# Optimization experiments

Hardware: AMD Instinct MI355X
Metric: run time of the kernel (lower is better)

Reference implementation:

```python
import jax, jax.numpy as jnp
import numpy as np
import math

H = 1024   # d_model
N = 64     # state size; N//2 complex modes
L_LEN = 4096


def setup_inputs() -> dict:
    key = jax.random.key(0)
    k1, k2 = jax.random.split(key)
    # S4D init: log_dt uniform in [log(dt_min), log(dt_max)]
    log_dt = jax.random.uniform(k1, (H,), dtype=jnp.float32) * (
        math.log(0.1) - math.log(0.001)) + math.log(0.001)
    # C complex, stored as real view (channels=1, H, N/2, 2)
    C_real = jax.random.normal(k2, (1, H, N // 2, 2), dtype=jnp.float32)
    log_A_real = jnp.log(0.5 * jnp.ones((H, N // 2), dtype=jnp.float32))
    A_imag = math.pi * jnp.tile(jnp.arange(N // 2, dtype=jnp.float32), (H, 1))
    return {"log_dt": log_dt, "C_real": C_real, "log_A_real": log_A_real,
            "A_imag": A_imag, "L": L_LEN}


def reference(log_dt, C_real, log_A_real, A_imag, L):
    # materialize_parms
    dt = jnp.exp(log_dt)                                  # (H,)
    A = -jnp.exp(log_A_real) + 1j * A_imag                # (H, N/2) complex
    C = C_real[..., 0] + 1j * C_real[..., 1]              # (1, H, N/2) complex
    # discretize (bilinear)
    dtA = A * dt[:, None]                                 # (H, N/2)
    B = dt[:, None] / (1.0 - dtA / 2)                     # (H, N/2)
    dC = C * B                                            # (1, H, N/2)
    dA = (1.0 + dtA / 2) / (1.0 - dtA / 2)                # (H, N/2)
    # log-Vandermonde: K[c,h,l] = 2*Re sum_n dC[c,h,n] * dA[h,n]**l
    x = jnp.log(dA)                                       # (H, N/2) complex
    ls = jnp.arange(L)                                    # (L,)
    V = jnp.exp(x[..., None] * ls)                        # (H, N/2, L) complex
    K = 2.0 * jnp.real(jnp.einsum('chn,hnl->chl', dC, V)) # (1, H, L)
    return K
```

## Files before the change

### kernel.cpp

```cpp
#include <hip/hip_runtime.h>
#include <math.h>

#define MODES 32
#define BLOCK 256
#define TWO_PI 6.283185307179586f
#define INV_2PI 0.15915494309189535f

__device__ __forceinline__ float rfl(float x) {
    return __int_as_float(__builtin_amdgcn_readfirstlane(__float_as_int(x)));
}

__global__ __launch_bounds__(BLOCK) void s4d_kernel(
    const float* __restrict__ log_dt,
    const float* __restrict__ C_real,
    const float* __restrict__ log_A_real,
    const float* __restrict__ A_imag,
    float* __restrict__ out,
    int L)
{
    const int h   = blockIdx.x;
    const int tid = threadIdx.x;
    const int P   = L / BLOCK;

    __shared__ float4 s_c0[MODES];
    __shared__ float4 s_c1[MODES];

    if (tid < MODES) {
        const int n = tid;
        const float dt = __expf(log_dt[h]);
        const float ar = -__expf(log_A_real[h * MODES + n]);
        const float ai = A_imag[h * MODES + n];
        const float dtAr = ar * dt, dtAi = ai * dt;
        const float den_r = 1.0f - 0.5f * dtAr, den_i = -0.5f * dtAi;
        const float num_r = 1.0f + 0.5f * dtAr, num_i =  0.5f * dtAi;
        const float inv = 1.0f / (den_r * den_r + den_i * den_i);
        const float Br =  dt * den_r * inv;
        const float Bi = -dt * den_i * inv;
        const float Cr = C_real[(h * MODES + n) * 2 + 0];
        const float Ci = C_real[(h * MODES + n) * 2 + 1];
        const float dCr = Cr * Br - Ci * Bi;
        const float dCi = Cr * Bi + Ci * Br;
        const float dAr = (num_r * den_r + num_i * den_i) * inv;
        const float dAi = (num_i * den_r - num_r * den_i) * inv;
        const float xr  = 0.5f * __logf(dAr * dAr + dAi * dAi);
        const float rev = atan2f(dAi, dAr) * INV_2PI;

        const float S   = (float)BLOCK;
        const float mag = __expf(xr * S);
        const float t   = rev * S;
        const float fr  = t - rintf(t);
        float ws, wc;
        __sincosf(fr * TWO_PI, &ws, &wc);
        const float wr = mag * wc, wi = mag * ws;

        s_c0[n] = make_float4(xr, rev, 2.0f * dCr, 2.0f * dCi);
        s_c1[n] = make_float4(wr, wi, 2.0f * wr, -(mag * mag));
    }
    __syncthreads();

    float m0[MODES], m1[MODES];
    float aS[MODES], bS[MODES];
    float acc0 = 0.0f, acc1 = 0.0f;
    const float lf = (float)tid;

    #pragma unroll
    for (int n = 0; n < MODES; ++n) {
        const float4 c0 = s_c0[n];
        const float4 c1 = s_c1[n];
        const float er = __expf(c0.x * lf);
        const float t  = c0.y * lf;
        const float fr = t - rintf(t);
        float sn, cs;
        __sincosf(fr * TWO_PI, &sn, &cs);
        const float pr = er * cs, pi = er * sn;
        const float v0 = fmaf(c0.z, pr, -c0.w * pi);
        const float qr = fmaf(pr, c1.x, -pi * c1.y);
        const float qi = fmaf(pr, c1.y,  pi * c1.x);
        const float v1 = fmaf(c0.z, qr, -c0.w * qi);
        m0[n] = v0; m1[n] = v1;
        acc0 += v0; acc1 += v1;
        aS[n] = rfl(c1.z);
        bS[n] = rfl(c1.w);
    }

    float* outp = out + (size_t)h * (size_t)L + tid;
    outp[0] = acc0;
    if (P > 1) outp[BLOCK] = acc1;

    int p = 2;
    for (; p + 1 < P; p += 2) {
        float accA = 0.0f, accB = 0.0f;
        #pragma unroll
        for (int n = 0; n < MODES; ++n) {
            const float mA = fmaf(aS[n], m1[n], bS[n] * m0[n]);
            const float mB = fmaf(aS[n], mA,    bS[n] * m1[n]);
            accA += mA; accB += mB;
            m0[n] = mA; m1[n] = mB;
        }
        outp[(size_t)p * BLOCK]       = accA;
        outp[(size_t)(p + 1) * BLOCK] = accB;
    }
    if (p < P) {
        float accA = 0.0f;
        #pragma unroll
        for (int n = 0; n < MODES; ++n) {
            const float mA = fmaf(aS[n], m1[n], bS[n] * m0[n]);
            accA += mA;
            m0[n] = m1[n]; m1[n] = mA;
        }
        outp[(size_t)p * BLOCK] = accA;
    }
}

extern "C" void kernel_launch(void* const* d_in, const int* in_sizes, int n_in,
                              void* d_out, int out_size, void* d_ws, size_t ws_size,
                              hipStream_t stream) {
    const float* log_dt     = (const float*)d_in[0];
    const float* C_real     = (const float*)d_in[1];
    const float* log_A_real = (const float*)d_in[2];
    const float* A_imag     = (const float*)d_in[3];
    float* out = (float*)d_out;

    const int H = in_sizes[0];
    const int L = out_size / H;

    s4d_kernel<<<H, BLOCK, 0, stream>>>(log_dt, C_real, log_A_real, A_imag, out, L);
}
```

Before: 78.62 us.

## Compute Vandermonde sum as split-bf16 MFMA GEMM factored over 64x64 positions

Writes each position l as 64*i+j, so that dA^l factors into dA^(64i) * dA^j. The kernel builds two 64x32 complex factor matrices in LDS and evaluates the mode sum as a small matrix multiply on MFMA bf16 instructions. A hi/lo bf16 split with three cross products stands in for fp32 precision. This replaces the per-thread serial second-order recurrence over L with a fixed amount of matrix-core work. The risk is lost accuracy from the bf16 splitting and the dropped lo*lo term. The old recurrence kernel stays as a fallback when L is not 4096.

New measurement: 71.18 us. 9.5% less time.

```diff
diff --git a/kernel.cpp b/kernel.cpp
--- a/kernel.cpp
+++ b/kernel.cpp
@@ -5,28 +5,44 @@
 #define BLOCK 256
 #define TWO_PI 6.283185307179586f
 #define INV_2PI 0.15915494309189535f
-
-__device__ __forceinline__ float rfl(float x) {
-    return __int_as_float(__builtin_amdgcn_readfirstlane(__float_as_int(x)));
-}
-
-__global__ __launch_bounds__(BLOCK) void s4d_kernel(
+#define LROWW 36
+
+typedef __attribute__((ext_vector_type(8))) short bf16x8;
+typedef __attribute__((ext_vector_type(4))) float f32x4;
+
+__device__ __forceinline__ void split2(float a, float b, unsigned int& hi, unsigned int& lo) {
+    unsigned int ua = __float_as_uint(a);
+    unsigned int ra = ua + 0x7FFFu + ((ua >> 16) & 1u);
+    unsigned int ub = __float_as_uint(b);
+    unsigned int rb = ub + 0x7FFFu + ((ub >> 16) & 1u);
+    float ha = __uint_as_float(ra & 0xFFFF0000u);
+    float hb = __uint_as_float(rb & 0xFFFF0000u);
+    float la = a - ha, lb = b - hb;
+    unsigned int ula = __float_as_uint(la); ula += 0x7FFFu + ((ula >> 16) & 1u);
+    unsigned int ulb = __float_as_uint(lb); ulb += 0x7FFFu + ((ulb >> 16) & 1u);
+    hi = (ra >> 16) | (rb & 0xFFFF0000u);
+    lo = (ula >> 16) | (ulb & 0xFFFF0000u);
+}
+
+__global__ __launch_bounds__(BLOCK) void s4d_mfma(
     const float* __restrict__ log_dt,
     const float* __restrict__ C_real,
     const float* __restrict__ log_A_real,
     const float* __restrict__ A_imag,
-    float* __restrict__ out,
-    int L)
+    float* __restrict__ out)
 {
-    const int h   = blockIdx.x;
-    const int tid = threadIdx.x;
-    const int P   = L / BLOCK;
-
-    __shared__ float4 s_c0[MODES];
-    __shared__ float4 s_c1[MODES];
-
-    if (tid < MODES) {
-        const int n = tid;
+    __shared__ __align__(16) unsigned int sAhi[64 * LROWW];
+    __shared__ __align__(16) unsigned int sAlo[64 * LROWW];
+    __shared__ __align__(16) unsigned int sBhi[64 * LROWW];
+    __shared__ __align__(16) unsigned int sBlo[64 * LROWW];
+    __shared__ float s_xr[MODES], s_rev[MODES], s_xr64[MODES], s_rev64[MODES];
+    __shared__ float s_dcr[MODES], s_dci[MODES];
+
+    const int h = blockIdx.x;
+    const int t = threadIdx.x;
+
+    if (t < MODES) {
+        const int n = t;
         const float dt = __expf(log_dt[h]);
         const float ar = -__expf(log_A_real[h * MODES + n]);
         const float ai = A_imag[h * MODES + n];
@@ -44,69 +60,156 @@
         const float dAi = (num_i * den_r - num_r * den_i) * inv;
         const float xr  = 0.5f * __logf(dAr * dAr + dAi * dAi);
         const float rev = atan2f(dAi, dAr) * INV_2PI;
-
-        const float S   = (float)BLOCK;
+        s_xr[n]  = xr;
+        s_rev[n] = rev;
+        s_xr64[n] = 64.0f * xr;
+        float r64 = 64.0f * rev; r64 -= rintf(r64);
+        s_rev64[n] = r64;
+        s_dcr[n] = 2.0f * dCr;
+        s_dci[n] = 2.0f * dCi;
+    }
+    __syncthreads();
+
+    {
+        const int mode = t & 31;
+        const int i8   = t >> 5;
+        const float xr = s_xr[mode], rev = s_rev[mode];
+        const float xr64 = s_xr64[mode], rev64 = s_rev64[mode];
+        const float dcr = s_dcr[mode], dci = s_dci[mode];
+        #pragma unroll
+        for (int b = 0; b < 8; ++b) {
+            const int idx = i8 + b * 8;
+            const float f = (float)idx;
+            const int word = idx * LROWW + mode;
+            {
+                const float er = __expf(xr * f);
+                float ph = rev * f; ph -= rintf(ph);
+                float sn, cs; __sincosf(ph * TWO_PI, &sn, &cs);
+                unsigned int hi, lo;
+                split2(er * cs, er * sn, hi, lo);
+                sBhi[word] = hi; sBlo[word] = lo;
+            }
+            {
+                const float mag = __expf(xr64 * f);
+                float ph = rev64 * f; ph -= rintf(ph);
+                float sn, cs; __sincosf(ph * TWO_PI, &sn, &cs);
+                const float wr = mag * cs, wi = mag * sn;
+                const float pr  = dcr * wr - dci * wi;
+                const float pi2 = dcr * wi + dci * wr;
+                unsigned int hi, lo;
+                split2(pr, -pi2, hi, lo);
+                sAhi[word] = hi; sAlo[word] = lo;
+            }
+        }
+    }
+    __syncthreads();
+
+    const int wv   = t >> 6;
+    const int lane = t & 63;
+    const int c16  = lane & 15;
+    const int quad = lane >> 4;
+
+    const int arow = (wv * 16 + c16) * LROWW + quad * 4;
+    const bf16x8 ah0 = *(const bf16x8*)&sAhi[arow];
+    const bf16x8 ah1 = *(const bf16x8*)&sAhi[arow + 16];
+    const bf16x8 al0 = *(const bf16x8*)&sAlo[arow];
+    const bf16x8 al1 = *(const bf16x8*)&sAlo[arow + 16];
+
+    float* op = out + ((size_t)h << 12) + (size_t)(wv * 16 + quad * 4) * 64 + c16;
+
+    #pragma unroll
+    for (int nt = 0; nt < 4; ++nt) {
+        const int brow = (nt * 16 + c16) * LROWW + quad * 4;
+        const bf16x8 bh0 = *(const bf16x8*)&sBhi[brow];
+        const bf16x8 bh1 = *(const bf16x8*)&sBhi[brow + 16];
+        const bf16x8 bl0 = *(const bf16x8*)&sBlo[brow];
+        const bf16x8 bl1 = *(const bf16x8*)&sBlo[brow + 16];
+
+        f32x4 acc = {0.f, 0.f, 0.f, 0.f};
+        acc = __builtin_amdgcn_mfma_f32_16x16x32_bf16(ah0, bh0, acc, 0, 0, 0);
+        acc = __builtin_amdgcn_mfma_f32_16x16x32_bf16(ah1, bh1, acc, 0, 0, 0);
+        acc = __builtin_amdgcn_mfma_f32_16x16x32_bf16(ah0, bl0, acc, 0, 0, 0);
+        acc = __builtin_amdgcn_mfma_f32_16x16x32_bf16(ah1, bl1, acc, 0, 0, 0);
+        acc = __builtin_amdgcn_mfma_f32_16x16x32_bf16(al0, bh0, acc, 0, 0, 0);
+        acc = __builtin_amdgcn_mfma_f32_16x16x32_bf16(al1, bh1, acc, 0, 0, 0);
+
+        #pragma unroll
+        for (int r = 0; r < 4; ++r)
+            op[(size_t)r * 64 + nt * 16] = acc[r];
+    }
+}
+
+__global__ __launch_bounds__(BLOCK) void s4d_recur(
+    const float* __restrict__ log_dt, const float* __restrict__ C_real,
+    const float* __restrict__ log_A_real, const float* __restrict__ A_imag,
+    float* __restrict__ out, int L)
+{
+    const int h = blockIdx.x, tid = threadIdx.x;
+    const int P = L / BLOCK;
+    __shared__ float4 s_c0[MODES], s_c1[MODES];
+    if (tid < MODES) {
+        const int n = tid;
+        const float dt = __expf(log_dt[h]);
+        const float ar = -__expf(log_A_real[h * MODES + n]);
+        const float ai = A_imag[h * MODES + n];
+        const float dtAr = ar * dt, dtAi = ai * dt;
+        const float den_r = 1.0f - 0.5f * dtAr, den_i = -0.5f * dtAi;
+        const float num_r = 1.0f + 0.5f * dtAr, num_i = 0.5f * dtAi;
+        const float inv = 1.0f / (den_r * den_r + den_i * den_i);
+        const float Brr = dt * den_r * inv, Bii = -dt * den_i * inv;
+        const float Cr = C_real[(h * MODES + n) * 2 + 0];
+        const float Ci = C_real[(h * MODES + n) * 2 + 1];
+        const float dCr = Cr * Brr - Ci * Bii, dCi = Cr * Bii + Ci * Brr;
+        const float dAr = (num_r * den_r + num_i * den_i) * inv;
+        const float dAi = (num_i * den_r - num_r * den_i) * inv;
+        const float xr = 0.5f * __logf(dAr * dAr + dAi * dAi);
+        const float rev = atan2f(dAi, dAr) * INV_2PI;
+        const float S = (float)BLOCK;
         const float mag = __expf(xr * S);
-        const float t   = rev * S;
-        const float fr  = t - rintf(t);
-        float ws, wc;
-        __sincosf(fr * TWO_PI, &ws, &wc);
-        const float wr = mag * wc, wi = mag * ws;
-
+        float tt = rev * S; tt -= rintf(tt);
+        float ws, wc; __sincosf(tt * TWO_PI, &ws, &wc);
         s_c0[n] = make_float4(xr, rev, 2.0f * dCr, 2.0f * dCi);
-        s_c1[n] = make_float4(wr, wi, 2.0f * wr, -(mag * mag));
+        s_c1[n] = make_float4(mag * wc, mag * ws, 2.0f * mag * wc, -(mag * mag));
     }
     __syncthreads();
-
-    float m0[MODES], m1[MODES];
-    float aS[MODES], bS[MODES];
-    float acc0 = 0.0f, acc1 = 0.0f;
+    float m0[MODES], m1[MODES], aS[MODES], bS[MODES];
+    float acc0 = 0.f, acc1 = 0.f;
     const float lf = (float)tid;
-
     #pragma unroll
     for (int n = 0; n < MODES; ++n) {
-        const float4 c0 = s_c0[n];
-        const float4 c1 = s_c1[n];
+        const float4 c0 = s_c0[n]; const float4 c1 = s_c1[n];
         const float er = __expf(c0.x * lf);
-        const float t  = c0.y * lf;
-        const float fr = t - rintf(t);
-        float sn, cs;
-        __sincosf(fr * TWO_PI, &sn, &cs);
+        float tt = c0.y * lf; tt -= rintf(tt);
+        float sn, cs; __sincosf(tt * TWO_PI, &sn, &cs);
         const float pr = er * cs, pi = er * sn;
         const float v0 = fmaf(c0.z, pr, -c0.w * pi);
         const float qr = fmaf(pr, c1.x, -pi * c1.y);
-        const float qi = fmaf(pr, c1.y,  pi * c1.x);
+        const float qi = fmaf(pr, c1.y, pi * c1.x);
         const float v1 = fmaf(c0.z, qr, -c0.w * qi);
-        m0[n] = v0; m1[n] = v1;
-        acc0 += v0; acc1 += v1;
-        aS[n] = rfl(c1.z);
-        bS[n] = rfl(c1.w);
-    }
-
+        m0[n] = v0; m1[n] = v1; acc0 += v0; acc1 += v1;
+        aS[n] = c1.z; bS[n] = c1.w;
+    }
     float* outp = out + (size_t)h * (size_t)L + tid;
     outp[0] = acc0;
     if (P > 1) outp[BLOCK] = acc1;
-
     int p = 2;
     for (; p + 1 < P; p += 2) {
-        float accA = 0.0f, accB = 0.0f;
+        float accA = 0.f, accB = 0.f;
         #pragma unroll
         for (int n = 0; n < MODES; ++n) {
             const float mA = fmaf(aS[n], m1[n], bS[n] * m0[n]);
-            const float mB = fmaf(aS[n], mA,    bS[n] * m1[n]);
-            accA += mA; accB += mB;
-            m0[n] = mA; m1[n] = mB;
+            const float mB = fmaf(aS[n], mA, bS[n] * m1[n]);
+            accA += mA; accB += mB; m0[n] = mA; m1[n] = mB;
         }
-        outp[(size_t)p * BLOCK]       = accA;
+        outp[(size_t)p * BLOCK] = accA;
         outp[(size_t)(p + 1) * BLOCK] = accB;
     }
     if (p < P) {
-        float accA = 0.0f;
+        float accA = 0.f;
         #pragma unroll
         for (int n = 0; n < MODES; ++n) {
             const float mA = fmaf(aS[n], m1[n], bS[n] * m0[n]);
-            accA += mA;
-            m0[n] = m1[n]; m1[n] = mA;
+            accA += mA; m0[n] = m1[n]; m1[n] = mA;
         }
         outp[(size_t)p * BLOCK] = accA;
     }
@@ -124,5 +227,9 @@
     const int H = in_sizes[0];
     const int L = out_size / H;
 
-    s4d_kernel<<<H, BLOCK, 0, stream>>>(log_dt, C_real, log_A_real, A_imag, out, L);
-}
+    if (L == 4096) {
+        s4d_mfma<<<H, BLOCK, 0, stream>>>(log_dt, C_real, log_A_real, A_imag, out);
+    } else {
+        s4d_recur<<<H, BLOCK, 0, stream>>>(log_dt, C_real, log_A_real, A_imag, out, L);
+    }
+}
```
